# Performance work log

Measured on AMD Instinct MI355X. Metric: run time of the kernel, lower is better.

## Reference

```python
import jax, jax.numpy as jnp
import numpy as np

N_IN = 100000
N_OUT = 50000
K = 32
E = N_OUT * K
CIN = 16
COUT = 32
KS = 4  # kernel_size per axis


def setup_inputs() -> dict:
    key = jax.random.key(0)
    ks = jax.random.split(key, 8)
    feats = jax.random.normal(ks[0], (N_IN, CIN), jnp.float32)
    inp_points = jax.random.uniform(ks[1], (N_IN, 3), jnp.float32)
    out_points = jax.random.uniform(ks[2], (N_OUT, 3), jnp.float32)
    # voxel size (extent) per output point
    out_extents = 0.1 + 0.1 * jax.random.uniform(ks[3], (N_OUT,), jnp.float32)
    scale_compat = jax.random.uniform(ks[4], (E,), jnp.float32)
    neighbors_index = jax.random.randint(ks[5], (E,), 0, N_IN, jnp.int32)
    # fixed-degree ragged structure: K neighbors per output voxel
    neighbors_row_splits = (jnp.arange(N_OUT + 1) * K).astype(jnp.int32)
    neighbors_distance = jax.random.uniform(ks[6], (E,), jnp.float32)
    kernel = 0.1 * jax.random.normal(ks[7], (KS, KS, KS, CIN, COUT), jnp.float32)
    bias = 0.01 * jax.random.normal(jax.random.fold_in(key, 99), (COUT,), jnp.float32)
    return dict(feats=feats, inp_points=inp_points, out_points=out_points,
                out_extents=out_extents, scale_compat=scale_compat,
                neighbors_index=neighbors_index,
                neighbors_row_splits=neighbors_row_splits,
                neighbors_distance=neighbors_distance, kernel=kernel, bias=bias)


def window_poly6(d):
    # poly6 smoothing window on normalized distance, clamped to [0,1]
    return jnp.clip((1.0 - d * d) ** 3, 0.0, 1.0)


def reference(feats, inp_points, out_points, out_extents, scale_compat,
              neighbors_index, neighbors_row_splits, neighbors_distance,
              kernel, bias):
    E_ = neighbors_index.shape[0]
    n_out = out_points.shape[0]
    cin = feats.shape[1]
    cout = kernel.shape[-1]
    nk = KS * KS * KS  # 64 kernel taps

    # per-edge output id from row_splits
    out_ids = jnp.searchsorted(neighbors_row_splits, jnp.arange(E_), side='right') - 1

    # per-neighbor importance = scale_compat * window_poly6(distance)
    imp = scale_compat * window_poly6(neighbors_distance)

    # relative position normalized to [-1,1] ball (extent is full voxel size)
    rel = (inp_points[neighbors_index] - out_points[out_ids]) / (0.5 * out_extents[out_ids])[:, None]

    # ball_to_cube_radial: radially stretch ball to cube, u = v * ||v||_2 / ||v||_inf
    r = jnp.sqrt(jnp.sum(rel * rel, axis=-1))
    linf = jnp.max(jnp.abs(rel), axis=-1)
    u = rel * (r / jnp.maximum(linf, 1e-12))[:, None]

    # trilinear interpolation coords in kernel grid [0, KS-1]
    t = jnp.clip((u * 0.5 + 0.5) * (KS - 1), 0.0, KS - 1.0)
    t0 = jnp.clip(jnp.floor(t), 0.0, KS - 2.0)
    f = t - t0                      # fractional part, [E,3]
    t0 = t0.astype(jnp.int32)

    # importance-weighted gathered features [E, Cin]
    fe = feats[neighbors_index] * imp[:, None]

    # scatter into per-output per-tap accumulator B [N_out*64, Cin]
    B = jnp.zeros((n_out * nk, cin), feats.dtype)
    for dx in (0, 1):
        wx = f[:, 0] if dx else 1.0 - f[:, 0]
        ix = t0[:, 0] + dx
        for dy in (0, 1):
            wy = f[:, 1] if dy else 1.0 - f[:, 1]
            iy = t0[:, 1] + dy
            for dz in (0, 1):
                wz = f[:, 2] if dz else 1.0 - f[:, 2]
                iz = t0[:, 2] + dz
                w = wx * wy * wz
                kflat = (ix * KS + iy) * KS + iz
                seg = out_ids * nk + kflat
                B = B + jax.ops.segment_sum(fe * w[:, None], seg, num_segments=n_out * nk)

    # contract taps with kernel: [n_out,64,cin] x [64,cin,cout] -> [n_out,cout]
    out = jnp.einsum('nkc,kcd->nd', B.reshape(n_out, nk, cin), kernel.reshape(nk, cin, cout))

    # normalize by summed importance per output point
    den = jax.ops.segment_sum(imp, out_ids, num_segments=n_out)
    out = out / jnp.where(den > 0, den, 1.0)[:, None]

    return jax.nn.relu(out + bias)
```

## Files before the change

kernel.cpp:

```cpp
#include <hip/hip_runtime.h>
#include <hip/hip_bf16.h>
#include <hip/hip_fp16.h>

#define NOUT 50000
#define KNB 32
#define CIN 16
#define COUT 32
#define NTAP 64
#define GP 8
#define ROW2B 2064

typedef __attribute__((ext_vector_type(8))) short short8;
typedef __attribute__((ext_vector_type(4))) float f32x4;

__device__ __forceinline__ unsigned int pk2(float lo, float hi) {
  union { __hip_bfloat162 h2; unsigned int u; } cv;
  cv.h2 = __float22bfloat162_rn(make_float2(lo, hi));
  return cv.u;
}
__device__ __forceinline__ unsigned int pkh(float lo, float hi) {
  union { __half2 h; unsigned int u; } cv;
  cv.h = __floats2half2_rn(lo, hi);
  return cv.u;
}
__device__ __forceinline__ unsigned int f2bf(float f) {
  unsigned int u = __float_as_uint(f);
  return (u + 0x7fffu + ((u >> 16) & 1u)) >> 16;
}

__global__ void prep_w_kernel(const float* __restrict__ kern,
                              unsigned short* __restrict__ wf) {
  int idx = blockIdx.x * 256 + threadIdx.x;
  if (idx >= NTAP * CIN * COUT) return;
  int j = idx & 7;
  int n = (idx >> 3) & 31;
  int g = (idx >> 8) & 3;
  int s = idx >> 10;
  int kc = s * 32 + g * 8 + j;
  wf[idx] = (unsigned short)f2bf(kern[kc * COUT + n]);
}

__launch_bounds__(256, 8)
__global__ void cconv_kernel(const float* __restrict__ feats,
                             const float* __restrict__ inp_points,
                             const float* __restrict__ out_points,
                             const float* __restrict__ out_extents,
                             const float* __restrict__ scale_compat,
                             const int* __restrict__ nidx,
                             const float* __restrict__ ndist,
                             const unsigned short* __restrict__ wf,
                             const float* __restrict__ bias,
                             float* __restrict__ out) {
  __shared__ __align__(16) char s_bl[GP * ROW2B];
  __shared__ uint2 s_edp[GP * KNB];
  __shared__ float s_cacc[GP][COUT];
  __shared__ float s_den[GP];

  const int tid = threadIdx.x;
  const int wv = tid >> 6;
  const int lane = tid & 63;
  const int c = lane & 15;
  const int g = lane >> 4;

  ((float*)s_cacc)[tid] = 0.0f;

  float fpre[2][8];
#pragma unroll
  for (int h = 0; h < 2; ++h) {
    const int pg = blockIdx.x * GP + wv * 2 + h;
#pragma unroll
    for (int j = 0; j < 8; ++j) {
      const int nb = nidx[pg * KNB + g * 8 + j];
      fpre[h][j] = feats[nb * CIN + c];
    }
  }

  {
    const int h = lane >> 5;
    const int e = lane & 31;
    const int p = wv * 2 + h;
    const int pg = blockIdx.x * GP + p;
    const int eg = pg * KNB + e;
    const int nb = nidx[eg];
    const float d = ndist[eg];
    float q = 1.0f - d * d;
    float w6 = q * q * q;
    w6 = fminf(fmaxf(w6, 0.0f), 1.0f);
    const float imp = scale_compat[eg] * w6;

    const float inv = 1.0f / (0.5f * out_extents[pg]);
    const float rx = (inp_points[nb * 3 + 0] - out_points[pg * 3 + 0]) * inv;
    const float ry = (inp_points[nb * 3 + 1] - out_points[pg * 3 + 1]) * inv;
    const float rz = (inp_points[nb * 3 + 2] - out_points[pg * 3 + 2]) * inv;
    const float r = sqrtf(rx * rx + ry * ry + rz * rz);
    const float linf = fmaxf(fabsf(rx), fmaxf(fabsf(ry), fabsf(rz)));
    const float sf = r / fmaxf(linf, 1e-12f);
    const float tx = fminf(fmaxf((rx * sf * 0.5f + 0.5f) * 3.0f, 0.0f), 3.0f);
    const float ty = fminf(fmaxf((ry * sf * 0.5f + 0.5f) * 3.0f, 0.0f), 3.0f);
    const float tz = fminf(fmaxf((rz * sf * 0.5f + 0.5f) * 3.0f, 0.0f), 3.0f);

    s_edp[p * KNB + e] = make_uint2(pkh(tx, ty), pkh(tz, imp));

    float dsum = imp;
#pragma unroll
    for (int m = 1; m < 32; m <<= 1) dsum += __shfl_xor(dsum, m);
    if (e == 0) s_den[p] = dsum;
  }

  {
    const float kyf = (float)(c >> 2);
    const float kzf = (float)(c & 3);
#pragma unroll
    for (int h = 0; h < 2; ++h) {
      const int p = wv * 2 + h;
      union { unsigned int u[4]; short8 v; } wfr0, wfr1, wfr2, wfr3, fef;
      float wprev0, wprev1, wprev2, wprev3, feprev;
#pragma unroll
      for (int j = 0; j < 8; ++j) {
        const uint2 ep = s_edp[p * KNB + g * 8 + j];
        union { unsigned int u; __half2 h2; } ua, ub;
        ua.u = ep.x; ub.u = ep.y;
        const float tx = __low2float(ua.h2), ty = __high2float(ua.h2);
        const float tz = __low2float(ub.h2), im = __high2float(ub.h2);
        const float f = fpre[h][j];
        const float hy = fmaxf(0.0f, 1.0f - fabsf(ty - kyf));
        const float hz = fmaxf(0.0f, 1.0f - fabsf(tz - kzf));
        const float m = hy * hz * im;
        const float w0 = fmaxf(0.0f, 1.0f - tx) * m;
        const float w1 = fmaxf(0.0f, 1.0f - fabsf(tx - 1.0f)) * m;
        const float w2 = fmaxf(0.0f, 1.0f - fabsf(tx - 2.0f)) * m;
        const float w3 = fmaxf(0.0f, tx - 2.0f) * m;
        if (j & 1) {
          wfr0.u[j >> 1] = pk2(wprev0, w0);
          wfr1.u[j >> 1] = pk2(wprev1, w1);
          wfr2.u[j >> 1] = pk2(wprev2, w2);
          wfr3.u[j >> 1] = pk2(wprev3, w3);
          fef.u[j >> 1] = pk2(feprev, f);
        } else {
          wprev0 = w0; wprev1 = w1; wprev2 = w2; wprev3 = w3; feprev = f;
        }
      }
      const f32x4 z = {0.f, 0.f, 0.f, 0.f};
      f32x4 d0 = __builtin_amdgcn_mfma_f32_16x16x32_bf16(fef.v, wfr0.v, z, 0, 0, 0);
      f32x4 d1 = __builtin_amdgcn_mfma_f32_16x16x32_bf16(fef.v, wfr1.v, z, 0, 0, 0);
      f32x4 d2 = __builtin_amdgcn_mfma_f32_16x16x32_bf16(fef.v, wfr2.v, z, 0, 0, 0);
      f32x4 d3 = __builtin_amdgcn_mfma_f32_16x16x32_bf16(fef.v, wfr3.v, z, 0, 0, 0);
      char* bp = s_bl + (unsigned)(p * ROW2B + c * 32 + g * 8);
      *(uint2*)(bp + 0 * 512) = make_uint2(pk2(d0[0], d0[1]), pk2(d0[2], d0[3]));
      *(uint2*)(bp + 1 * 512) = make_uint2(pk2(d1[0], d1[1]), pk2(d1[2], d1[3]));
      *(uint2*)(bp + 2 * 512) = make_uint2(pk2(d2[0], d2[1]), pk2(d2[2], d2[3]));
      *(uint2*)(bp + 3 * 512) = make_uint2(pk2(d3[0], d3[1]), pk2(d3[2], d3[3]));
    }
  }

  __syncthreads();

  f32x4 acc0 = {0.f, 0.f, 0.f, 0.f}, acc1 = {0.f, 0.f, 0.f, 0.f};
  const int pl = lane & 15;
  const int arow = pl & (GP - 1);
  const int g4 = lane >> 4;
#pragma unroll
  for (int ss = 0; ss < 8; ++ss) {
    const int s = wv * 8 + ss;
    const short8 a = *(const short8*)(s_bl + arow * ROW2B + s * 64 + g4 * 16);
    const short8 b0 = *(const short8*)(wf + ((unsigned)((s * 4 + g4) * 32) + pl) * 8);
    const short8 b1 = *(const short8*)(wf + ((unsigned)((s * 4 + g4) * 32) + 16 + pl) * 8);
    acc0 = __builtin_amdgcn_mfma_f32_16x16x32_bf16(a, b0, acc0, 0, 0, 0);
    acc1 = __builtin_amdgcn_mfma_f32_16x16x32_bf16(a, b1, acc1, 0, 0, 0);
  }
#pragma unroll
  for (int j = 0; j < 4; ++j) {
    const int row = g4 * 4 + j;
    if (row < GP) {
      atomicAdd(&s_cacc[row][pl], acc0[j]);
      atomicAdd(&s_cacc[row][pl + 16], acc1[j]);
    }
  }

  __syncthreads();

  {
    const int p = tid >> 5;
    const int dch = tid & 31;
    const float den = s_den[p];
    float v = ((float*)s_cacc)[tid] / (den > 0.0f ? den : 1.0f) + bias[dch];
    out[blockIdx.x * (GP * COUT) + tid] = fmaxf(v, 0.0f);
  }
}

extern "C" void kernel_launch(void* const* d_in, const int* in_sizes, int n_in,
                              void* d_out, int out_size, void* d_ws, size_t ws_size,
                              hipStream_t stream) {
  const float* feats        = (const float*)d_in[0];
  const float* inp_points   = (const float*)d_in[1];
  const float* out_points   = (const float*)d_in[2];
  const float* out_extents  = (const float*)d_in[3];
  const float* scale_compat = (const float*)d_in[4];
  const int*   nidx         = (const int*)d_in[5];
  const float* ndist        = (const float*)d_in[7];
  const float* kern         = (const float*)d_in[8];
  const float* bias         = (const float*)d_in[9];
  unsigned short* wf = (unsigned short*)d_ws;

  prep_w_kernel<<<(NTAP * CIN * COUT + 255) / 256, 256, 0, stream>>>(kern, wf);
  cconv_kernel<<<NOUT / GP, 256, 0, stream>>>(feats, inp_points, out_points,
                                              out_extents, scale_compat, nidx,
                                              ndist, wf, bias, (float*)d_out);
}
```

Before: 68.76 us.

## Switch MFMA path to fp16 with packed half2 weight math and shuffled neighbor indices

```diff
diff --git a/kernel.cpp b/kernel.cpp
--- a/kernel.cpp
+++ b/kernel.cpp
@@ -1,5 +1,4 @@
 #include <hip/hip_runtime.h>
-#include <hip/hip_bf16.h>
 #include <hip/hip_fp16.h>
 
 #define NOUT 50000
@@ -10,22 +9,22 @@
 #define GP 8
 #define ROW2B 2064
 
-typedef __attribute__((ext_vector_type(8))) short short8;
+typedef __attribute__((ext_vector_type(8))) _Float16 half8;
+typedef __attribute__((ext_vector_type(2))) _Float16 h2v;
 typedef __attribute__((ext_vector_type(4))) float f32x4;
 
-__device__ __forceinline__ unsigned int pk2(float lo, float hi) {
-  union { __hip_bfloat162 h2; unsigned int u; } cv;
-  cv.h2 = __float22bfloat162_rn(make_float2(lo, hi));
-  return cv.u;
+__device__ __forceinline__ h2v pmax(h2v a, h2v b) {
+  h2v d;
+  asm("v_pk_max_f16 %0, %1, %2" : "=v"(d) : "v"(a), "v"(b));
+  return d;
 }
 __device__ __forceinline__ unsigned int pkh(float lo, float hi) {
   union { __half2 h; unsigned int u; } cv;
   cv.h = __floats2half2_rn(lo, hi);
   return cv.u;
 }
-__device__ __forceinline__ unsigned int f2bf(float f) {
-  unsigned int u = __float_as_uint(f);
-  return (u + 0x7fffu + ((u >> 16) & 1u)) >> 16;
+__device__ __forceinline__ unsigned short f2hbits(float f) {
+  union { __half h; unsigned short s; } c; c.h = __float2half_rn(f); return c.s;
 }
 
 __global__ void prep_w_kernel(const float* __restrict__ kern,
@@ -37,7 +36,7 @@
   int g = (idx >> 8) & 3;
   int s = idx >> 10;
   int kc = s * 32 + g * 8 + j;
-  wf[idx] = (unsigned short)f2bf(kern[kc * COUT + n]);
+  wf[idx] = f2hbits(kern[kc * COUT + n]);
 }
 
 __launch_bounds__(256, 8)
@@ -52,7 +51,10 @@
                              const float* __restrict__ bias,
                              float* __restrict__ out) {
   __shared__ __align__(16) char s_bl[GP * ROW2B];
-  __shared__ uint2 s_edp[GP * KNB];
+  __shared__ __align__(4) unsigned short s_tx[GP * KNB];
+  __shared__ __align__(4) unsigned short s_ty[GP * KNB];
+  __shared__ __align__(4) unsigned short s_tz[GP * KNB];
+  __shared__ __align__(4) unsigned short s_im[GP * KNB];
   __shared__ float s_cacc[GP][COUT];
   __shared__ float s_den[GP];
 
@@ -64,13 +66,13 @@
 
   ((float*)s_cacc)[tid] = 0.0f;
 
+  const int my_nb = nidx[blockIdx.x * (GP * KNB) + tid];
   float fpre[2][8];
 #pragma unroll
   for (int h = 0; h < 2; ++h) {
-    const int pg = blockIdx.x * GP + wv * 2 + h;
 #pragma unroll
     for (int j = 0; j < 8; ++j) {
-      const int nb = nidx[pg * KNB + g * 8 + j];
+      const int nb = __shfl(my_nb, h * 32 + g * 8 + j);
       fpre[h][j] = feats[nb * CIN + c];
     }
   }
@@ -81,7 +83,7 @@
     const int p = wv * 2 + h;
     const int pg = blockIdx.x * GP + p;
     const int eg = pg * KNB + e;
-    const int nb = nidx[eg];
+    const int nb = my_nb;
     const float d = ndist[eg];
     float q = 1.0f - d * d;
     float w6 = q * q * q;
@@ -99,7 +101,10 @@
     const float ty = fminf(fmaxf((ry * sf * 0.5f + 0.5f) * 3.0f, 0.0f), 3.0f);
     const float tz = fminf(fmaxf((rz * sf * 0.5f + 0.5f) * 3.0f, 0.0f), 3.0f);
 
-    s_edp[p * KNB + e] = make_uint2(pkh(tx, ty), pkh(tz, imp));
+    s_tx[tid] = f2hbits(tx);
+    s_ty[tid] = f2hbits(ty);
+    s_tz[tid] = f2hbits(tz);
+    s_im[tid] = f2hbits(imp);
 
     float dsum = imp;
 #pragma unroll
@@ -108,48 +113,55 @@
   }
 
   {
-    const float kyf = (float)(c >> 2);
-    const float kzf = (float)(c & 3);
+    const _Float16 kys = (_Float16)(short)(c >> 2);
+    const _Float16 kzs = (_Float16)(short)(c & 3);
+    const h2v z2 = {(_Float16)0, (_Float16)0};
+    const h2v one2 = {(_Float16)1, (_Float16)1};
+    const h2v two2 = {(_Float16)2, (_Float16)2};
+    const h2v ky2 = {kys, kys};
+    const h2v kz2 = {kzs, kzs};
 #pragma unroll
     for (int h = 0; h < 2; ++h) {
       const int p = wv * 2 + h;
-      union { unsigned int u[4]; short8 v; } wfr0, wfr1, wfr2, wfr3, fef;
-      float wprev0, wprev1, wprev2, wprev3, feprev;
-#pragma unroll
-      for (int j = 0; j < 8; ++j) {
-        const uint2 ep = s_edp[p * KNB + g * 8 + j];
-        union { unsigned int u; __half2 h2; } ua, ub;
-        ua.u = ep.x; ub.u = ep.y;
-        const float tx = __low2float(ua.h2), ty = __high2float(ua.h2);
-        const float tz = __low2float(ub.h2), im = __high2float(ub.h2);
-        const float f = fpre[h][j];
-        const float hy = fmaxf(0.0f, 1.0f - fabsf(ty - kyf));
-        const float hz = fmaxf(0.0f, 1.0f - fabsf(tz - kzf));
-        const float m = hy * hz * im;
-        const float w0 = fmaxf(0.0f, 1.0f - tx) * m;
-        const float w1 = fmaxf(0.0f, 1.0f - fabsf(tx - 1.0f)) * m;
-        const float w2 = fmaxf(0.0f, 1.0f - fabsf(tx - 2.0f)) * m;
-        const float w3 = fmaxf(0.0f, tx - 2.0f) * m;
-        if (j & 1) {
-          wfr0.u[j >> 1] = pk2(wprev0, w0);
-          wfr1.u[j >> 1] = pk2(wprev1, w1);
-          wfr2.u[j >> 1] = pk2(wprev2, w2);
-          wfr3.u[j >> 1] = pk2(wprev3, w3);
-          fef.u[j >> 1] = pk2(feprev, f);
-        } else {
-          wprev0 = w0; wprev1 = w1; wprev2 = w2; wprev3 = w3; feprev = f;
-        }
+      union { unsigned int u[4]; h2v h[4]; half8 v; } wfr0, wfr1, wfr2, wfr3, fef;
+#pragma unroll
+      for (int jp = 0; jp < 4; ++jp) {
+        const int eb = p * KNB + g * 8 + jp * 2;
+        const h2v tx2 = *(const h2v*)&s_tx[eb];
+        const h2v ty2 = *(const h2v*)&s_ty[eb];
+        const h2v tz2 = *(const h2v*)&s_tz[eb];
+        const h2v im2 = *(const h2v*)&s_im[eb];
+        h2v t = ty2 - ky2;
+        h2v at = pmax(t, z2 - t);
+        const h2v hy = pmax(z2, one2 - at);
+        t = tz2 - kz2;
+        at = pmax(t, z2 - t);
+        const h2v hz = pmax(z2, one2 - at);
+        const h2v m2 = hy * hz * im2;
+        const h2v w0 = pmax(z2, one2 - tx2) * m2;
+        t = tx2 - one2;
+        at = pmax(t, z2 - t);
+        const h2v w1 = pmax(z2, one2 - at) * m2;
+        t = tx2 - two2;
+        at = pmax(t, z2 - t);
+        const h2v w2 = pmax(z2, one2 - at) * m2;
+        const h2v w3 = pmax(z2, t) * m2;
+        wfr0.h[jp] = w0;
+        wfr1.h[jp] = w1;
+        wfr2.h[jp] = w2;
+        wfr3.h[jp] = w3;
+        fef.u[jp] = pkh(fpre[h][jp * 2], fpre[h][jp * 2 + 1]);
       }
       const f32x4 z = {0.f, 0.f, 0.f, 0.f};
-      f32x4 d0 = __builtin_amdgcn_mfma_f32_16x16x32_bf16(fef.v, wfr0.v, z, 0, 0, 0);
-      f32x4 d1 = __builtin_amdgcn_mfma_f32_16x16x32_bf16(fef.v, wfr1.v, z, 0, 0, 0);
-      f32x4 d2 = __builtin_amdgcn_mfma_f32_16x16x32_bf16(fef.v, wfr2.v, z, 0, 0, 0);
-      f32x4 d3 = __builtin_amdgcn_mfma_f32_16x16x32_bf16(fef.v, wfr3.v, z, 0, 0, 0);
+      f32x4 d0 = __builtin_amdgcn_mfma_f32_16x16x32_f16(fef.v, wfr0.v, z, 0, 0, 0);
+      f32x4 d1 = __builtin_amdgcn_mfma_f32_16x16x32_f16(fef.v, wfr1.v, z, 0, 0, 0);
+      f32x4 d2 = __builtin_amdgcn_mfma_f32_16x16x32_f16(fef.v, wfr2.v, z, 0, 0, 0);
+      f32x4 d3 = __builtin_amdgcn_mfma_f32_16x16x32_f16(fef.v, wfr3.v, z, 0, 0, 0);
       char* bp = s_bl + (unsigned)(p * ROW2B + c * 32 + g * 8);
-      *(uint2*)(bp + 0 * 512) = make_uint2(pk2(d0[0], d0[1]), pk2(d0[2], d0[3]));
-      *(uint2*)(bp + 1 * 512) = make_uint2(pk2(d1[0], d1[1]), pk2(d1[2], d1[3]));
-      *(uint2*)(bp + 2 * 512) = make_uint2(pk2(d2[0], d2[1]), pk2(d2[2], d2[3]));
-      *(uint2*)(bp + 3 * 512) = make_uint2(pk2(d3[0], d3[1]), pk2(d3[2], d3[3]));
+      *(uint2*)(bp + 0 * 512) = make_uint2(pkh(d0[0], d0[1]), pkh(d0[2], d0[3]));
+      *(uint2*)(bp + 1 * 512) = make_uint2(pkh(d1[0], d1[1]), pkh(d1[2], d1[3]));
+      *(uint2*)(bp + 2 * 512) = make_uint2(pkh(d2[0], d2[1]), pkh(d2[2], d2[3]));
+      *(uint2*)(bp + 3 * 512) = make_uint2(pkh(d3[0], d3[1]), pkh(d3[2], d3[3]));
     }
   }
 
@@ -162,11 +174,11 @@
 #pragma unroll
   for (int ss = 0; ss < 8; ++ss) {
     const int s = wv * 8 + ss;
-    const short8 a = *(const short8*)(s_bl + arow * ROW2B + s * 64 + g4 * 16);
-    const short8 b0 = *(const short8*)(wf + ((unsigned)((s * 4 + g4) * 32) + pl) * 8);
-    const short8 b1 = *(const short8*)(wf + ((unsigned)((s * 4 + g4) * 32) + 16 + pl) * 8);
-    acc0 = __builtin_amdgcn_mfma_f32_16x16x32_bf16(a, b0, acc0, 0, 0, 0);
-    acc1 = __builtin_amdgcn_mfma_f32_16x16x32_bf16(a, b1, acc1, 0, 0, 0);
+    const half8 a = *(const half8*)(s_bl + arow * ROW2B + s * 64 + g4 * 16);
+    const half8 b0 = *(const half8*)(wf + ((unsigned)((s * 4 + g4) * 32) + pl) * 8);
+    const half8 b1 = *(const half8*)(wf + ((unsigned)((s * 4 + g4) * 32) + 16 + pl) * 8);
+    acc0 = __builtin_amdgcn_mfma_f32_16x16x32_f16(a, b0, acc0, 0, 0, 0);
+    acc1 = __builtin_amdgcn_mfma_f32_16x16x32_f16(a, b1, acc1, 0, 0, 0);
   }
 #pragma unroll
   for (int j = 0; j < 4; ++j) {
```

Measured after the change: 68.96 us. No clear change (+0.3%).
